# Performance work log

Measured on AMD Instinct MI355X. Metric: run time of the kernel, lower is better.

## Reference

```python
import jax, jax.numpy as jnp
import numpy as np
import math

B, N, K, H = 2, 2048, 1024, 16
S = K // H  # head dim = 64


def apply_rope(t):
    # t: [b, h, N, s] -> rotary position embedding (rotate-half convention)
    s = t.shape[-1]
    pos = jnp.arange(t.shape[2], dtype=jnp.float32)
    inv_freq = 1.0 / (10000.0 ** (jnp.arange(0, s, 2, dtype=jnp.float32) / s))
    ang = pos[:, None] * inv_freq[None, :]               # [N, s/2]
    cos = jnp.concatenate([jnp.cos(ang), jnp.cos(ang)], axis=-1)  # [N, s]
    sin = jnp.concatenate([jnp.sin(ang), jnp.sin(ang)], axis=-1)
    t1, t2 = t[..., : s // 2], t[..., s // 2:]
    rot = jnp.concatenate([-t2, t1], axis=-1)
    return t * cos + rot * sin


def setup_inputs() -> dict:
    key = jax.random.key(0)
    ks = jax.random.split(key, 6)
    sc = 1.0 / math.sqrt(K)
    x = jax.random.normal(ks[0], (B, N, K), dtype=jnp.float32)
    Wq = jax.random.normal(ks[1], (K, K), dtype=jnp.float32) * sc
    Wk = jax.random.normal(ks[2], (K, K), dtype=jnp.float32) * sc
    Wv = jax.random.normal(ks[3], (K, K), dtype=jnp.float32) * sc
    Wu = jax.random.normal(ks[4], (K, K), dtype=jnp.float32) * sc
    bu = jax.random.normal(ks[5], (K,), dtype=jnp.float32) * 0.01
    mask = jnp.tril(jnp.ones((N, N), dtype=jnp.int32))  # causal
    return {"x": x, "Wq": Wq, "Wk": Wk, "Wv": Wv, "Wu": Wu, "bu": bu, "mask": mask}


def reference(x, Wq, Wk, Wv, Wu, bu, mask):
    b, n, k = x.shape
    h, s = H, S
    # torch Linear: y = x @ W.T
    def proj(W):
        return (x @ W.T).reshape(b, n, h, s).transpose(0, 2, 1, 3)  # [b,h,n,s]
    Q = apply_rope(proj(Wq))
    Kh = apply_rope(proj(Wk))
    V = proj(Wv)
    scores = jnp.einsum('bhqs,bhks->bhqk', Q, Kh) / math.sqrt(s)
    scores = jnp.where(mask[None, None, :, :] == 0, -jnp.inf, scores)
    attn = jax.nn.softmax(scores, axis=-1)
    out = jnp.einsum('bhqk,bhks->bhqs', attn, V)           # [b,h,n,s]
    out = out.transpose(0, 2, 1, 3).reshape(b, n, k)
    return out @ Wu.T + bu
```

## Files before the change

### kernel.cpp

```cpp
#include <hip/hip_runtime.h>
#include <hip/hip_bf16.h>

#define Bq 2
#define Nq 2048
#define Kq 1024
#define Hq 16
#define Sq 64
#define Mq (Bq * Nq)

typedef __attribute__((ext_vector_type(4))) float f32x4;
typedef __attribute__((ext_vector_type(8))) short bf16x8;

__device__ unsigned short g_xb[(size_t)Mq * Kq];
__device__ unsigned short g_Wqb[Kq * Kq];
__device__ unsigned short g_Wkb[Kq * Kq];
__device__ unsigned short g_Wvb[Kq * Kq];
__device__ unsigned short g_Wub[Kq * Kq];
__device__ unsigned short g_Qb[(size_t)Bq * Hq * Nq * Sq];
__device__ unsigned short g_Kb[(size_t)Bq * Hq * Nq * Sq];
__device__ unsigned short g_Vt[(size_t)Bq * Hq * Sq * Nq];
__device__ unsigned short g_Ao[(size_t)Mq * Kq];
__device__ __align__(16) float g_On[(size_t)32 * 16 * 3 * 128 * 64];
__device__ float g_Ol[32 * 16 * 3 * 128];

__constant__ signed char c_qt[30] = {15,15,15,14,14,14,13,13,13,12,12,12,11,11,10,10,9,9,8,8,7,7,6,6,5,4,3,2,1,0};
__constant__ signed char c_t0[30] = {0,6,11,0,5,10,0,5,10,0,5,9,0,6,0,6,0,5,0,5,0,4,0,4,0,0,0,0,0,0};
__constant__ signed char c_t1[30] = {6,11,16,5,10,15,5,10,14,5,9,13,6,12,6,11,5,10,5,9,4,8,4,7,6,5,4,3,2,1};
__constant__ signed char c_sp[30] = {0,1,2,0,1,2,0,1,2,0,1,2,0,1,0,1,0,1,0,1,0,1,0,1,0,0,0,0,0,0};
__constant__ signed char c_ns[30] = {3,3,3,3,3,3,3,3,3,3,3,3,2,2,2,2,2,2,2,2,2,2,2,2,1,1,1,1,1,1};

__device__ __forceinline__ unsigned short f2bf(float f) {
    union { float f; unsigned int i; } u; u.f = f;
    unsigned int r = u.i + 0x7FFF + ((u.i >> 16) & 1);
    return (unsigned short)(r >> 16);
}
__device__ __forceinline__ float bf2f(unsigned short u) {
    union { unsigned int i; float f; } v; v.i = ((unsigned int)u) << 16;
    return v.f;
}
__device__ __forceinline__ void async16(const unsigned short* g, unsigned short* l) {
    __builtin_amdgcn_global_load_lds(
        (const __attribute__((address_space(1))) void*)g,
        (__attribute__((address_space(3))) void*)l, 16, 0, 0);
}

__global__ __launch_bounds__(256) void convert_all_kernel(
    const float* __restrict__ x,  const float* __restrict__ wq,
    const float* __restrict__ wk, const float* __restrict__ wv,
    const float* __restrict__ wu)
{
    int i = blockIdx.x * 256 + threadIdx.x;
    const float* src; unsigned short* dst; int off;
    if (i < 1048576) { src = x; dst = g_xb; off = i; }
    else {
        int j = i - 1048576;
        int which = j >> 18;
        off = j & 262143;
        src = (which == 0) ? wq : (which == 1) ? wk : (which == 2) ? wv : wu;
        dst = (which == 0) ? g_Wqb : (which == 1) ? g_Wkb : (which == 2) ? g_Wvb : g_Wub;
    }
    float4 v = ((const float4*)src)[off];
    ushort4 o;
    o.x = f2bf(v.x); o.y = f2bf(v.y); o.z = f2bf(v.z); o.w = f2bf(v.w);
    ((ushort4*)dst)[off] = o;
}

__global__ __launch_bounds__(512, 2) void qkv_gemm_kernel()
{
    __shared__ __align__(16) unsigned short SLDS[65536];
    auto As = (unsigned short (*)[256][64])(SLDS);
    auto Bs = (unsigned short (*)[256][64])(SLDS + 32768);

    const int n0 = blockIdx.x * 256;
    const int m0 = blockIdx.y * 256;
    const int which = n0 >> 10;
    const unsigned short* A  = g_xb;
    const unsigned short* Bm = (which == 0) ? g_Wqb : (which == 1) ? g_Wkb : g_Wvb;
    const int nb = n0 & 1023;

    const int tid = threadIdx.x;
    const int w = tid >> 6, l = tid & 63;
    const int lane16 = l & 15, quad = l >> 4;
    const int wr = w >> 2, wc = w & 3;
    const int sr8 = l >> 3;
    const int sc  = ((l & 7) ^ sr8) * 8;
    const int rsw = lane16 & 7;

    f32x4 acc[8][4];
#pragma unroll
    for (int mf = 0; mf < 8; ++mf)
#pragma unroll
        for (int nf = 0; nf < 4; ++nf) acc[mf][nf] = (f32x4){0.f, 0.f, 0.f, 0.f};

#define STG_A(t, b, c) async16(A  + (size_t)(m0 + (c)*64 + w*8 + sr8) * Kq + (t)*64 + sc, \
                               &As[(b)][(c)*64 + w*8][0])
#define STG_B(t, b, c) async16(Bm + (size_t)(nb + (c)*64 + w*8 + sr8) * Kq + (t)*64 + sc, \
                               &Bs[(b)][(c)*64 + w*8][0])

    STG_B(0, 0, 0); STG_B(0, 0, 1); STG_B(0, 0, 2); STG_B(0, 0, 3);
    STG_A(0, 0, 0); STG_A(0, 0, 2); STG_A(0, 0, 1); STG_A(0, 0, 3);
    asm volatile("s_waitcnt vmcnt(2)" ::: "memory");
    __builtin_amdgcn_s_barrier();

    int cur = 0;
    for (int t = 0; t < 16; ++t) {
        const bool stg = (t + 1 < 16);
        const int nxt = cur ^ 1;
        bf16x8 bf[4][2];
#pragma unroll
        for (int q = 0; q < 4; ++q) {
            asm volatile("" ::: "memory");
            bf16x8 af[2][2];
            if (q == 0) {
#pragma unroll
                for (int nf = 0; nf < 4; ++nf)
#pragma unroll
                    for (int ks = 0; ks < 2; ++ks)
                        bf[nf][ks] = *(const bf16x8*)
                            &Bs[cur][wc * 64 + nf * 16 + lane16][((ks * 4 + quad) ^ rsw) * 8];
            }
#pragma unroll
            for (int m2 = 0; m2 < 2; ++m2)
#pragma unroll
                for (int ks = 0; ks < 2; ++ks)
                    af[m2][ks] = *(const bf16x8*)
                        &As[cur][wr * 128 + (q * 2 + m2) * 16 + lane16][((ks * 4 + quad) ^ rsw) * 8];
            if (stg) {
                if (q == 0) { STG_B(t + 1, nxt, 0); STG_B(t + 1, nxt, 1); }
                if (q == 1) { STG_B(t + 1, nxt, 2); STG_B(t + 1, nxt, 3); }
                if (q == 2) { STG_A(t + 1, nxt, 0); STG_A(t + 1, nxt, 2); }
                if (q == 3) { STG_A(t + 1, nxt, 1); STG_A(t + 1, nxt, 3); }
            }
            asm volatile("" ::: "memory");
            __builtin_amdgcn_s_barrier();
            asm volatile("s_waitcnt lgkmcnt(0)" ::: "memory");
            __builtin_amdgcn_sched_barrier(0);
            __builtin_amdgcn_s_setprio(1);
#pragma unroll
            for (int m2 = 0; m2 < 2; ++m2)
#pragma unroll
                for (int nf = 0; nf < 4; ++nf)
#pragma unroll
                    for (int ks = 0; ks < 2; ++ks)
                        acc[q * 2 + m2][nf] = __builtin_amdgcn_mfma_f32_16x16x32_bf16(
                            af[m2][ks], bf[nf][ks], acc[q * 2 + m2][nf], 0, 0, 0);
            __builtin_amdgcn_s_setprio(0);
            if (q == 1) {
                if (stg) asm volatile("s_waitcnt vmcnt(4)" ::: "memory");
                else     asm volatile("s_waitcnt vmcnt(0)" ::: "memory");
            }
            if (q == 3) {
                if (stg) asm volatile("s_waitcnt vmcnt(2)" ::: "memory");
                else     asm volatile("s_waitcnt vmcnt(0)" ::: "memory");
            }
            __builtin_amdgcn_s_barrier();
        }
        cur ^= 1;
    }
#undef STG_A
#undef STG_B

    const int h0q = nb >> 6;
    if (which < 2) {
        unsigned short* dst = (which == 0) ? g_Qb : g_Kb;
        const int h = h0q + wc;
        const float invf0 = exp2f((float)lane16 * -0.41524101f);
        const float invf1 = exp2f((float)(lane16 + 16) * -0.41524101f);
#pragma unroll
        for (int mf = 0; mf < 8; ++mf)
#pragma unroll
            for (int r = 0; r < 4; ++r) {
                int m = m0 + wr * 128 + mf * 16 + quad * 4 + r;
                int b = m >> 11, nn = m & 2047;
                float np = (float)nn;
                float a0 = np * invf0, a1 = np * invf1;
                float s0 = __sinf(a0), c0 = __cosf(a0);
                float s1 = __sinf(a1), c1 = __cosf(a1);
                float t10 = acc[mf][0][r], t20 = acc[mf][2][r];
                float t11 = acc[mf][1][r], t21 = acc[mf][3][r];
                unsigned short* dr = dst + (((size_t)b * Hq + h) * Nq + nn) * Sq + lane16;
                dr[0]  = f2bf(t10 * c0 - t20 * s0);
                dr[16] = f2bf(t11 * c1 - t21 * s1);
                dr[32] = f2bf(t20 * c0 + t10 * s0);
                dr[48] = f2bf(t21 * c1 + t11 * s1);
            }
    } else {
        unsigned short* T = SLDS;
        const int b = m0 >> 11, mcol = m0 & 2047;
#pragma unroll
        for (int pass = 0; pass < 2; ++pass) {
            __syncthreads();
            if (wr == pass) {
#pragma unroll
                for (int mf = 0; mf < 8; ++mf)
#pragma unroll
                    for (int nf = 0; nf < 4; ++nf)
#pragma unroll
                        for (int r = 0; r < 4; ++r)
                            T[(wc * 64 + nf * 16 + lane16) * 136 + mf * 16 + quad * 4 + r] =
                                f2bf(acc[mf][nf][r]);
            }
            __syncthreads();
            {
                int row = tid >> 1;
                int h = h0q + (row >> 6), s = row & 63;
                unsigned short* drow = g_Vt + (((size_t)b * Hq + h) * Sq + s) * Nq
                                        + mcol + pass * 128 + (tid & 1) * 64;
                const unsigned short* srow = T + row * 136 + (tid & 1) * 64;
#pragma unroll
                for (int jj = 0; jj < 8; ++jj)
                    *(uint4*)(drow + jj * 8) = *(const uint4*)(srow + jj * 8);
            }
        }
    }
}

__global__ __launch_bounds__(512) void attn_kernel()
{
    const int bh = blockIdx.x;
    const int y  = blockIdx.y;
    const int qt  = c_qt[y];
    const int t0  = c_t0[y];
    const int t1  = c_t1[y];
    const int sp  = c_sp[y];
    const int nsp = c_ns[y];
    const int q0 = qt * 128;
    const unsigned short* Qp = g_Qb + (size_t)bh * Nq * Sq;
    const unsigned short* Kp = g_Kb + (size_t)bh * Nq * Sq;
    const unsigned short* Vp = g_Vt + (size_t)bh * Sq * Nq;

    __shared__ __align__(16) unsigned short Ks[2][2][64][64];
    __shared__ __align__(16) unsigned short Vs[2][2][64][64];
    __shared__ __align__(16) unsigned short Ps[128][64];
    unsigned short* psf = &Ps[0][0];

    const int tid = threadIdx.x;
    const int w = tid >> 6, l = tid & 63;
    const int lane16 = l & 15, quad = l >> 4;
    const int sr = l >> 3;
    const int sc = ((l & 7) ^ sr) * 8;
    const int rsw = (lane16 & 7);

    bf16x8 be;
    {
        short o = (lane16 == 0) ? (short)0x3F80 : (short)0;
#pragma unroll
        for (int i = 0; i < 8; ++i) be[i] = o;
    }

    const int qlo = q0 + 16 * w;
    bf16x8 aq0 = *(const bf16x8*)(Qp + (size_t)(qlo + lane16) * Sq + quad * 8);
    bf16x8 aq1 = *(const bf16x8*)(Qp + (size_t)(qlo + lane16) * Sq + quad * 8 + 32);
    asm volatile("" : "+v"(aq0), "+v"(aq1));

    f32x4 Oacc[4];
    f32x4 Oext = (f32x4){0.f, 0.f, 0.f, 0.f};
#pragma unroll
    for (int ds = 0; ds < 4; ++ds) Oacc[ds] = (f32x4){0.f, 0.f, 0.f, 0.f};

    const float C1 = 0.18033688f;
    const float C2 = 11.54156036f;

#define STAGE(t, b)                                                              \
    do {                                                                         \
        int kn_ = (t) * 128;                                                     \
        async16(Kp + (size_t)(kn_ + 8 * w + sr) * Sq + sc,      &Ks[(b)][0][8 * w][0]); \
        async16(Kp + (size_t)(kn_ + 64 + 8 * w + sr) * Sq + sc, &Ks[(b)][1][8 * w][0]); \
        async16(Vp + (size_t)(8 * w + sr) * Nq + kn_ + sc,      &Vs[(b)][0][8 * w][0]); \
        async16(Vp + (size_t)(8 * w + sr) * Nq + kn_ + 64 + sc, &Vs[(b)][1][8 * w][0]); \
    } while (0)

    STAGE(t0, 0);
    asm volatile("s_waitcnt vmcnt(0)" ::: "memory");
    __builtin_amdgcn_s_barrier();
    __builtin_amdgcn_sched_barrier(0);

    int cur = 0;
    for (int kb = t0; kb < t1; ++kb) {
        if (kb + 1 < t1) STAGE(kb + 1, cur ^ 1);

#pragma unroll
        for (int hh = 0; hh < 2; ++hh) {
            const int kbase = kb * 128 + hh * 64;
            if (kbase <= qlo + 15) {
                f32x4 S[4];
#pragma unroll
                for (int kc = 0; kc < 4; ++kc) S[kc] = (f32x4){0.f, 0.f, 0.f, 0.f};
#pragma unroll
                for (int kc = 0; kc < 4; ++kc) {
                    const unsigned short* krow = &Ks[cur][hh][kc * 16 + lane16][0];
                    bf16x8 bk0 = *(const bf16x8*)&krow[(quad ^ rsw) * 8];
                    bf16x8 bk1 = *(const bf16x8*)&krow[((4 + quad) ^ rsw) * 8];
                    S[kc] = __builtin_amdgcn_mfma_f32_16x16x32_bf16(aq0, bk0, S[kc], 0, 0, 0);
                    S[kc] = __builtin_amdgcn_mfma_f32_16x16x32_bf16(aq1, bk1, S[kc], 0, 0, 0);
                }

                const int qbase = qlo + quad * 4;
                if (kbase + 63 > qlo) {
#pragma unroll
                    for (int kc = 0; kc < 4; ++kc) {
                        int kpos = kbase + kc * 16 + lane16;
#pragma unroll
                        for (int r = 0; r < 4; ++r)
                            S[kc][r] = (kpos <= qbase + r) ? exp2f(fmaf(S[kc][r], C1, -C2)) : 0.0f;
                    }
                } else {
#pragma unroll
                    for (int kc = 0; kc < 4; ++kc)
#pragma unroll
                        for (int r = 0; r < 4; ++r)
                            S[kc][r] = exp2f(fmaf(S[kc][r], C1, -C2));
                }

#pragma unroll
                for (int kc = 0; kc < 4; ++kc)
#pragma unroll
                    for (int r = 0; r < 4; ++r) {
                        int prow = 16 * w + quad * 4 + r;
                        psf[(prow * 64 + kc * 16 + lane16) ^ ((prow & 7) << 3)] =
                            (unsigned short)(__float_as_uint(S[kc][r]) >> 16);
                    }

                const int prow2 = 16 * w + lane16;
#pragma unroll
                for (int kk = 0; kk < 2; ++kk) {
                    bf16x8 pa = *(const bf16x8*)(psf +
                        ((prow2 * 64 + kk * 32 + quad * 8) ^ (rsw << 3)));
#pragma unroll
                    for (int ds = 0; ds < 4; ++ds) {
                        bf16x8 vb = *(const bf16x8*)&Vs[cur][hh][ds * 16 + lane16][((kk * 4 + quad) ^ rsw) * 8];
                        Oacc[ds] = __builtin_amdgcn_mfma_f32_16x16x32_bf16(pa, vb, Oacc[ds], 0, 0, 0);
                    }
                    Oext = __builtin_amdgcn_mfma_f32_16x16x32_bf16(pa, be, Oext, 0, 0, 0);
                }
            }
        }

        __builtin_amdgcn_sched_barrier(0);
        asm volatile("s_waitcnt vmcnt(0)" ::: "memory");
        __builtin_amdgcn_s_barrier();
        __builtin_amdgcn_sched_barrier(0);
        cur ^= 1;
    }
#undef STAGE

    if (nsp == 1) {
        const int b = bh >> 4, h = bh & 15;
        float inv[4];
#pragma unroll
        for (int r = 0; r < 4; ++r) {
            float lr = __shfl(Oext[r], quad * 16, 64);
            inv[r] = 1.0f / lr;
        }
#pragma unroll
        for (int ds = 0; ds < 4; ++ds)
#pragma unroll
            for (int r = 0; r < 4; ++r) {
                int nn = qlo + quad * 4 + r;
                g_Ao[((size_t)b * Nq + nn) * Kq + h * Sq + ds * 16 + lane16] =
                    f2bf(Oacc[ds][r] * inv[r]);
            }
    } else {
        float* On = g_On + (((size_t)bh * 16 + qt) * 3 + sp) * (128 * 64);
        float* Ol = g_Ol + (((size_t)bh * 16 + qt) * 3 + sp) * 128;
#pragma unroll
        for (int r = 0; r < 4; ++r) {
            float lr = __shfl(Oext[r], quad * 16, 64);
            if (lane16 == 0) Ol[16 * w + quad * 4 + r] = lr;
        }
#pragma unroll
        for (int ds = 0; ds < 4; ++ds)
#pragma unroll
            for (int r = 0; r < 4; ++r)
                On[(16 * w + quad * 4 + r) * 64 + ds * 16 + lane16] = Oacc[ds][r];
    }
}

__global__ __launch_bounds__(256) void attn_combine_kernel()
{
    const int bh = blockIdx.x;
    const int qt = 6 + blockIdx.y;
    const int nsp = (qt >= 12) ? 3 : 2;
    const int tid = threadIdx.x;
    const int row = tid >> 1;
    const int ch  = (tid & 1) * 32;
    const size_t sb = ((size_t)bh * 16 + qt) * 3;
    const float* On0 = g_On + (sb + 0) * (128 * 64);
    const float* On1 = g_On + (sb + 1) * (128 * 64);
    const float* On2 = g_On + (sb + 2) * (128 * 64);
    const float* Ol  = g_Ol + sb * 128;

    float lsum = Ol[row] + Ol[128 + row];
    if (nsp == 3) lsum += Ol[256 + row];
    float inv = 1.0f / lsum;

    const int b = bh >> 4, h = bh & 15, nn = qt * 128 + row;
    unsigned short* dst = g_Ao + ((size_t)b * Nq + nn) * Kq + h * Sq + ch;

#pragma unroll
    for (int j = 0; j < 8; ++j) {
        int o = row * 64 + ch + j * 4;
        f32x4 v = *(const f32x4*)(On0 + o);
        v += *(const f32x4*)(On1 + o);
        if (nsp == 3) v += *(const f32x4*)(On2 + o);
        ushort4 u;
        u.x = f2bf(v[0] * inv); u.y = f2bf(v[1] * inv);
        u.z = f2bf(v[2] * inv); u.w = f2bf(v[3] * inv);
        ((ushort4*)dst)[j] = u;
    }
}

__global__ __launch_bounds__(512, 1) void out_gemm_kernel(
    const float* __restrict__ bu, float* __restrict__ out)
{
    __shared__ __align__(16) unsigned short SLDS[49152];
    auto As = (unsigned short (*)[256][64])(SLDS);
    auto Bs = (unsigned short (*)[128][64])(SLDS + 32768);

    const int n0 = blockIdx.x * 128;
    const int m0 = blockIdx.y * 256;

    const int tid = threadIdx.x;
    const int w = tid >> 6, l = tid & 63;
    const int lane16 = l & 15, quad = l >> 4;
    const int wr = w >> 2, wc = w & 3;
    const int sr8 = l >> 3;
    const int sc  = ((l & 7) ^ sr8) * 8;
    const int rsw = lane16 & 7;

    f32x4 acc[8][2];
#pragma unroll
    for (int mf = 0; mf < 8; ++mf)
#pragma unroll
        for (int nf = 0; nf < 2; ++nf) acc[mf][nf] = (f32x4){0.f, 0.f, 0.f, 0.f};

#define OST_A(t, b, c) async16(g_Ao  + (size_t)(m0 + (c)*64 + w*8 + sr8) * Kq + (t)*64 + sc, \
                               &As[(b)][(c)*64 + w*8][0])
#define OST_B(t, b, c) async16(g_Wub + (size_t)(n0 + (c)*64 + w*8 + sr8) * Kq + (t)*64 + sc, \
                               &Bs[(b)][(c)*64 + w*8][0])

    OST_B(0, 0, 0); OST_B(0, 0, 1);
    OST_A(0, 0, 0); OST_A(0, 0, 2);
    OST_A(0, 0, 1); OST_A(0, 0, 3);
    asm volatile("s_waitcnt vmcnt(2)" ::: "memory");
    __builtin_amdgcn_s_barrier();

    int cur = 0;
    for (int t = 0; t < 16; ++t) {
        const bool stg = (t + 1 < 16);
        const int nxt = cur ^ 1;
        bf16x8 bf[2][2];
#pragma unroll
        for (int q = 0; q < 4; ++q) {
            asm volatile("" ::: "memory");
            bf16x8 af[2][2];
            if (q == 0) {
#pragma unroll
                for (int nf = 0; nf < 2; ++nf)
#pragma unroll
                    for (int ks = 0; ks < 2; ++ks)
                        bf[nf][ks] = *(const bf16x8*)
                            &Bs[cur][wc * 32 + nf * 16 + lane16][((ks * 4 + quad) ^ rsw) * 8];
            }
#pragma unroll
            for (int m2 = 0; m2 < 2; ++m2)
#pragma unroll
                for (int ks = 0; ks < 2; ++ks)
                    af[m2][ks] = *(const bf16x8*)
                        &As[cur][wr * 128 + (q * 2 + m2) * 16 + lane16][((ks * 4 + quad) ^ rsw) * 8];
            if (stg) {
                if (q == 0) { OST_B(t + 1, nxt, 0); OST_B(t + 1, nxt, 1); }
                if (q == 1) { OST_A(t + 1, nxt, 0); OST_A(t + 1, nxt, 2); }
                if (q == 2) { OST_A(t + 1, nxt, 1); OST_A(t + 1, nxt, 3); }
            }
            asm volatile("" ::: "memory");
            __builtin_amdgcn_s_barrier();
            asm volatile("s_waitcnt lgkmcnt(0)" ::: "memory");
            __builtin_amdgcn_sched_barrier(0);
            __builtin_amdgcn_s_setprio(1);
#pragma unroll
            for (int m2 = 0; m2 < 2; ++m2)
#pragma unroll
                for (int nf = 0; nf < 2; ++nf)
#pragma unroll
                    for (int ks = 0; ks < 2; ++ks)
                        acc[q * 2 + m2][nf] = __builtin_amdgcn_mfma_f32_16x16x32_bf16(
                            af[m2][ks], bf[nf][ks], acc[q * 2 + m2][nf], 0, 0, 0);
            __builtin_amdgcn_s_setprio(0);
            if (q == 1) {
                if (stg) asm volatile("s_waitcnt vmcnt(4)" ::: "memory");
                else     asm volatile("s_waitcnt vmcnt(0)" ::: "memory");
            }
            if (q == 3) {
                if (stg) asm volatile("s_waitcnt vmcnt(2)" ::: "memory");
                else     asm volatile("s_waitcnt vmcnt(0)" ::: "memory");
            }
            __builtin_amdgcn_s_barrier();
        }
        cur ^= 1;
    }
#undef OST_A
#undef OST_B

#pragma unroll
    for (int mf = 0; mf < 8; ++mf)
#pragma unroll
        for (int nf = 0; nf < 2; ++nf)
#pragma unroll
            for (int r = 0; r < 4; ++r) {
                int m = m0 + wr * 128 + mf * 16 + quad * 4 + r;
                int n = n0 + wc * 32 + nf * 16 + lane16;
                out[(size_t)m * Kq + n] = acc[mf][nf][r] + bu[n];
            }
}

extern "C" void kernel_launch(void* const* d_in, const int* in_sizes, int n_in,
                              void* d_out, int out_size, void* d_ws, size_t ws_size,
                              hipStream_t stream)
{
    const float* x  = (const float*)d_in[0];
    const float* Wq = (const float*)d_in[1];
    const float* Wk = (const float*)d_in[2];
    const float* Wv = (const float*)d_in[3];
    const float* Wu = (const float*)d_in[4];
    const float* bu = (const float*)d_in[5];
    float* out = (float*)d_out;

    convert_all_kernel<<<8192, 256, 0, stream>>>(x, Wq, Wk, Wv, Wu);
    qkv_gemm_kernel<<<dim3(12, 16), 512, 0, stream>>>();
    attn_kernel<<<dim3(32, 30), 512, 0, stream>>>();
    attn_combine_kernel<<<dim3(32, 10), 256, 0, stream>>>();
    out_gemm_kernel<<<dim3(8, 16), 512, 0, stream>>>(bu, out);
}
```

Before: 211.5 us.

## Load K and V directly from global memory instead of LDS double-buffering

```diff
diff --git a/kernel.cpp b/kernel.cpp
--- a/kernel.cpp
+++ b/kernel.cpp
@@ -229,16 +229,12 @@
     const unsigned short* Kp = g_Kb + (size_t)bh * Nq * Sq;
     const unsigned short* Vp = g_Vt + (size_t)bh * Sq * Nq;
 
-    __shared__ __align__(16) unsigned short Ks[2][2][64][64];
-    __shared__ __align__(16) unsigned short Vs[2][2][64][64];
     __shared__ __align__(16) unsigned short Ps[128][64];
     unsigned short* psf = &Ps[0][0];
 
     const int tid = threadIdx.x;
     const int w = tid >> 6, l = tid & 63;
     const int lane16 = l & 15, quad = l >> 4;
-    const int sr = l >> 3;
-    const int sc = ((l & 7) ^ sr) * 8;
     const int rsw = (lane16 & 7);
 
     bf16x8 be;
@@ -251,7 +247,6 @@
     const int qlo = q0 + 16 * w;
     bf16x8 aq0 = *(const bf16x8*)(Qp + (size_t)(qlo + lane16) * Sq + quad * 8);
     bf16x8 aq1 = *(const bf16x8*)(Qp + (size_t)(qlo + lane16) * Sq + quad * 8 + 32);
-    asm volatile("" : "+v"(aq0), "+v"(aq1));
 
     f32x4 Oacc[4];
     f32x4 Oext = (f32x4){0.f, 0.f, 0.f, 0.f};
@@ -261,88 +256,64 @@
     const float C1 = 0.18033688f;
     const float C2 = 11.54156036f;
 
-#define STAGE(t, b)                                                              \
-    do {                                                                         \
-        int kn_ = (t) * 128;                                                     \
-        async16(Kp + (size_t)(kn_ + 8 * w + sr) * Sq + sc,      &Ks[(b)][0][8 * w][0]); \
-        async16(Kp + (size_t)(kn_ + 64 + 8 * w + sr) * Sq + sc, &Ks[(b)][1][8 * w][0]); \
-        async16(Vp + (size_t)(8 * w + sr) * Nq + kn_ + sc,      &Vs[(b)][0][8 * w][0]); \
-        async16(Vp + (size_t)(8 * w + sr) * Nq + kn_ + 64 + sc, &Vs[(b)][1][8 * w][0]); \
-    } while (0)
-
-    STAGE(t0, 0);
-    asm volatile("s_waitcnt vmcnt(0)" ::: "memory");
-    __builtin_amdgcn_s_barrier();
-    __builtin_amdgcn_sched_barrier(0);
-
-    int cur = 0;
-    for (int kb = t0; kb < t1; ++kb) {
-        if (kb + 1 < t1) STAGE(kb + 1, cur ^ 1);
-
-#pragma unroll
-        for (int hh = 0; hh < 2; ++hh) {
-            const int kbase = kb * 128 + hh * 64;
-            if (kbase <= qlo + 15) {
-                f32x4 S[4];
-#pragma unroll
-                for (int kc = 0; kc < 4; ++kc) S[kc] = (f32x4){0.f, 0.f, 0.f, 0.f};
-#pragma unroll
-                for (int kc = 0; kc < 4; ++kc) {
-                    const unsigned short* krow = &Ks[cur][hh][kc * 16 + lane16][0];
-                    bf16x8 bk0 = *(const bf16x8*)&krow[(quad ^ rsw) * 8];
-                    bf16x8 bk1 = *(const bf16x8*)&krow[((4 + quad) ^ rsw) * 8];
-                    S[kc] = __builtin_amdgcn_mfma_f32_16x16x32_bf16(aq0, bk0, S[kc], 0, 0, 0);
-                    S[kc] = __builtin_amdgcn_mfma_f32_16x16x32_bf16(aq1, bk1, S[kc], 0, 0, 0);
-                }
-
-                const int qbase = qlo + quad * 4;
-                if (kbase + 63 > qlo) {
-#pragma unroll
-                    for (int kc = 0; kc < 4; ++kc) {
-                        int kpos = kbase + kc * 16 + lane16;
-#pragma unroll
-                        for (int r = 0; r < 4; ++r)
-                            S[kc][r] = (kpos <= qbase + r) ? exp2f(fmaf(S[kc][r], C1, -C2)) : 0.0f;
-                    }
-                } else {
-#pragma unroll
-                    for (int kc = 0; kc < 4; ++kc)
-#pragma unroll
-                        for (int r = 0; r < 4; ++r)
-                            S[kc][r] = exp2f(fmaf(S[kc][r], C1, -C2));
-                }
-
-#pragma unroll
-                for (int kc = 0; kc < 4; ++kc)
-#pragma unroll
-                    for (int r = 0; r < 4; ++r) {
-                        int prow = 16 * w + quad * 4 + r;
-                        psf[(prow * 64 + kc * 16 + lane16) ^ ((prow & 7) << 3)] =
-                            (unsigned short)(__float_as_uint(S[kc][r]) >> 16);
-                    }
-
-                const int prow2 = 16 * w + lane16;
-#pragma unroll
-                for (int kk = 0; kk < 2; ++kk) {
-                    bf16x8 pa = *(const bf16x8*)(psf +
-                        ((prow2 * 64 + kk * 32 + quad * 8) ^ (rsw << 3)));
-#pragma unroll
-                    for (int ds = 0; ds < 4; ++ds) {
-                        bf16x8 vb = *(const bf16x8*)&Vs[cur][hh][ds * 16 + lane16][((kk * 4 + quad) ^ rsw) * 8];
-                        Oacc[ds] = __builtin_amdgcn_mfma_f32_16x16x32_bf16(pa, vb, Oacc[ds], 0, 0, 0);
-                    }
-                    Oext = __builtin_amdgcn_mfma_f32_16x16x32_bf16(pa, be, Oext, 0, 0, 0);
-                }
-            }
-        }
-
-        __builtin_amdgcn_sched_barrier(0);
-        asm volatile("s_waitcnt vmcnt(0)" ::: "memory");
-        __builtin_amdgcn_s_barrier();
-        __builtin_amdgcn_sched_barrier(0);
-        cur ^= 1;
-    }
-#undef STAGE
+    const int kb_end = 2 * t1;
+    for (int kb = 2 * t0; kb < kb_end; ++kb) {
+        const int kbase = kb * 64;
+        if (kbase > qlo + 15) continue;
+
+        const unsigned short* Kt = Kp + (size_t)kbase * Sq;
+        f32x4 S[4];
+#pragma unroll
+        for (int kc = 0; kc < 4; ++kc) S[kc] = (f32x4){0.f, 0.f, 0.f, 0.f};
+#pragma unroll
+        for (int kc = 0; kc < 4; ++kc) {
+            const unsigned short* krow = Kt + (size_t)(kc * 16 + lane16) * Sq;
+            bf16x8 bk0 = *(const bf16x8*)(krow + quad * 8);
+            bf16x8 bk1 = *(const bf16x8*)(krow + 32 + quad * 8);
+            S[kc] = __builtin_amdgcn_mfma_f32_16x16x32_bf16(aq0, bk0, S[kc], 0, 0, 0);
+            S[kc] = __builtin_amdgcn_mfma_f32_16x16x32_bf16(aq1, bk1, S[kc], 0, 0, 0);
+        }
+
+        const int qbase = qlo + quad * 4;
+        if (kbase + 63 > qlo) {
+#pragma unroll
+            for (int kc = 0; kc < 4; ++kc) {
+                int kpos = kbase + kc * 16 + lane16;
+#pragma unroll
+                for (int r = 0; r < 4; ++r)
+                    S[kc][r] = (kpos <= qbase + r) ? exp2f(fmaf(S[kc][r], C1, -C2)) : 0.0f;
+            }
+        } else {
+#pragma unroll
+            for (int kc = 0; kc < 4; ++kc)
+#pragma unroll
+                for (int r = 0; r < 4; ++r)
+                    S[kc][r] = exp2f(fmaf(S[kc][r], C1, -C2));
+        }
+
+#pragma unroll
+        for (int kc = 0; kc < 4; ++kc)
+#pragma unroll
+            for (int r = 0; r < 4; ++r) {
+                int prow = 16 * w + quad * 4 + r;
+                psf[(prow * 64 + kc * 16 + lane16) ^ ((prow & 7) << 3)] =
+                    (unsigned short)(__float_as_uint(S[kc][r]) >> 16);
+            }
+
+        const int prow2 = 16 * w + lane16;
+#pragma unroll
+        for (int kk = 0; kk < 2; ++kk) {
+            bf16x8 pa = *(const bf16x8*)(psf +
+                ((prow2 * 64 + kk * 32 + quad * 8) ^ (rsw << 3)));
+#pragma unroll
+            for (int ds = 0; ds < 4; ++ds) {
+                bf16x8 vb = *(const bf16x8*)(Vp +
+                    (size_t)(ds * 16 + lane16) * Nq + kbase + kk * 32 + quad * 8);
+                Oacc[ds] = __builtin_amdgcn_mfma_f32_16x16x32_bf16(pa, vb, Oacc[ds], 0, 0, 0);
+            }
+            Oext = __builtin_amdgcn_mfma_f32_16x16x32_bf16(pa, be, Oext, 0, 0, 0);
+        }
+    }
 
     if (nsp == 1) {
         const int b = bh >> 4, h = bh & 15;
```

Result: slower. 315.8 us (+49.3%).
